# Kernel tuning notes

Measured on AMD Instinct MI355X. Metric: run time of the kernel, lower is better.

The kernel has to match this reference:

```python
import jax, jax.numpy as jnp
import numpy as np

N_IN = 1048576
C = 64
VT_OUT = 262144


def setup_inputs() -> dict:
    key = jax.random.key(0)
    k1, k2, k3 = jax.random.split(key, 3)
    inputs = jax.random.normal(k1, (N_IN, C), dtype=jnp.float32)
    # per-vertex replacement counts (used as weights in avg pooling)
    vt_replace = jax.random.randint(k2, (N_IN,), 0, 4, dtype=jnp.int64)
    # map each input vertex to its decimated output vertex
    vt_map = jax.random.randint(k3, (N_IN,), 0, VT_OUT, dtype=jnp.int64)
    return {"inputs": inputs, "vt_replace": vt_replace, "vt_map": vt_map, "vt_out": VT_OUT}


def reference(inputs, vt_replace, vt_map, vt_out):
    # method == 'max': segmented max over groups of input vertices that
    # collapse onto the same output vertex. vt_map < 0 means the vertex is
    # dropped; route those to an extra trash segment and slice it off.
    valid = vt_map >= 0
    seg = jnp.where(valid, vt_map, vt_out)  # [N_in]
    out = jax.ops.segment_max(inputs, seg, num_segments=vt_out + 1)[:vt_out]
    # empty segments come back as -inf; zero them like the CUDA kernel's init
    return jnp.where(jnp.isneginf(out), jnp.zeros((), dtype=out.dtype), out)
```

## Files before the change

kernel.cpp:

```cpp
#include <hip/hip_runtime.h>


#define CCH 64
#define NEG_INF (-__builtin_huge_valf())

__global__ void head_init_kernel(int* __restrict__ head, int vt_out) {
    int i = blockIdx.x * blockDim.x + threadIdx.x;
    if (i < vt_out) head[i] = -1;
}

__global__ void list_build_kernel(const int* __restrict__ vt_map,
                                  int* __restrict__ head,
                                  int* __restrict__ next,
                                  int n_in, int vt_out) {
    int r = blockIdx.x * blockDim.x + threadIdx.x;
    if (r >= n_in) return;
    int seg = vt_map[r];
    if (seg < 0 || seg >= vt_out) return;
    next[r] = atomicExch(&head[seg], r);
}

__global__ void gather_max_kernel(const float* __restrict__ in,
                                  const int* __restrict__ head,
                                  const int* __restrict__ next,
                                  float* __restrict__ out, int vt_out) {
    int wave = blockIdx.x * 4 + (threadIdx.x >> 6);
    int lane = threadIdx.x & 63;
    if (wave >= vt_out) return;
    int r = head[wave];
    float m = NEG_INF;
    while (r >= 0) {
        m = fmaxf(m, in[(size_t)r * CCH + lane]);
        r = next[r];
    }
    out[(size_t)wave * CCH + lane] = (m == NEG_INF) ? 0.0f : m;
}

__device__ __forceinline__ unsigned enc_f32(float f) {
    unsigned u = __float_as_uint(f);
    return (u & 0x80000000u) ? ~u : (u | 0x80000000u);
}
__device__ __forceinline__ float dec_f32(unsigned u) {
    unsigned b = (u & 0x80000000u) ? (u & 0x7fffffffu) : ~u;
    return __uint_as_float(b);
}
static constexpr unsigned ENC_NEG_INF = 0x007FFFFFu;

__global__ void pool_init_kernel(uint4* __restrict__ out, int n4) {
    int i = blockIdx.x * blockDim.x + threadIdx.x;
    if (i < n4) out[i] = make_uint4(ENC_NEG_INF, ENC_NEG_INF, ENC_NEG_INF, ENC_NEG_INF);
}
__global__ void pool_scatter_kernel(const float4* __restrict__ in,
                                    const int* __restrict__ vt_map,
                                    unsigned* __restrict__ out,
                                    int n_in, int vt_out) {
    int t = blockIdx.x * blockDim.x + threadIdx.x;
    int row = t >> 4, g = t & 15;
    if (row >= n_in) return;
    int seg = vt_map[row];
    if (seg < 0 || seg >= vt_out) return;
    float4 v = in[row * 16 + g];
    unsigned* dst = out + (size_t)seg * CCH + g * 4;
    atomicMax(dst + 0, enc_f32(v.x));
    atomicMax(dst + 1, enc_f32(v.y));
    atomicMax(dst + 2, enc_f32(v.z));
    atomicMax(dst + 3, enc_f32(v.w));
}
__global__ void pool_decode_kernel(uint4* __restrict__ out, int n4) {
    int i = blockIdx.x * blockDim.x + threadIdx.x;
    if (i >= n4) return;
    uint4 u = out[i];
    float4 f;
    f.x = (u.x == ENC_NEG_INF) ? 0.0f : dec_f32(u.x);
    f.y = (u.y == ENC_NEG_INF) ? 0.0f : dec_f32(u.y);
    f.z = (u.z == ENC_NEG_INF) ? 0.0f : dec_f32(u.z);
    f.w = (u.w == ENC_NEG_INF) ? 0.0f : dec_f32(u.w);
    ((float4*)out)[i] = f;
}

extern "C" void kernel_launch(void* const* d_in, const int* in_sizes, int n_in_arr,
                              void* d_out, int out_size, void* d_ws, size_t ws_size,
                              hipStream_t stream) {
    const float* in     = (const float*)d_in[0];
    const int*   vt_map = (const int*)d_in[2];
    float*       out    = (float*)d_out;

    const int n_in   = in_sizes[0] / CCH;
    const int vt_out = out_size / CCH;
    const int B = 256;

    const size_t ws_needed = (size_t)(vt_out + n_in) * sizeof(int);
    if (ws_size >= ws_needed) {
        int* head = (int*)d_ws;
        int* next = head + vt_out;
        head_init_kernel<<<(vt_out + B - 1) / B, B, 0, stream>>>(head, vt_out);
        list_build_kernel<<<(n_in + B - 1) / B, B, 0, stream>>>(
            vt_map, head, next, n_in, vt_out);
        const int waves = vt_out;
        gather_max_kernel<<<(waves + 3) / 4, B, 0, stream>>>(
            in, head, next, out, vt_out);
    } else {
        unsigned* out_u = (unsigned*)d_out;
        const int n4 = out_size / 4;
        pool_init_kernel<<<(n4 + B - 1) / B, B, 0, stream>>>((uint4*)out_u, n4);
        pool_scatter_kernel<<<(n_in * 16 + B - 1) / B, B, 0, stream>>>(
            (const float4*)in, vt_map, out_u, n_in, vt_out);
        pool_decode_kernel<<<(n4 + B - 1) / B, B, 0, stream>>>((uint4*)out_u, n4);
    }
}
```

Measured before the change: 489.2 us.

## Replace linked-list segment gather with CSR build and batched row loads

```diff
diff --git a/kernel.cpp b/kernel.cpp
--- a/kernel.cpp
+++ b/kernel.cpp
@@ -4,14 +4,120 @@
 #define CCH 64
 #define NEG_INF (-__builtin_huge_valf())
 
+
+__global__ void zero_kernel(int* __restrict__ p, int n) {
+    int i = blockIdx.x * blockDim.x + threadIdx.x;
+    if (i < n) p[i] = 0;
+}
+
+__global__ void count_kernel(const int* __restrict__ vt_map,
+                             int* __restrict__ cnt,
+                             int* __restrict__ rank,
+                             int n_in, int vt_out) {
+    int r = blockIdx.x * blockDim.x + threadIdx.x;
+    if (r >= n_in) return;
+    int seg = vt_map[r];
+    if (seg < 0 || seg >= vt_out) { rank[r] = -1; return; }
+    rank[r] = atomicAdd(&cnt[seg], 1);
+}
+
+__global__ void bsum_kernel(const int* __restrict__ cnt, int* __restrict__ bs,
+                            int vt_out) {
+    __shared__ int s[256];
+    int b = blockIdx.x, t = threadIdx.x, i = b * 256 + t;
+    s[t] = (i < vt_out) ? cnt[i] : 0;
+    __syncthreads();
+    for (int d = 128; d > 0; d >>= 1) {
+        if (t < d) s[t] += s[t + d];
+        __syncthreads();
+    }
+    if (t == 0) bs[b] = s[0];
+}
+
+__global__ void scan_bs_kernel(int* __restrict__ bs, int n) {
+    __shared__ int s[1024];
+    int t = threadIdx.x;
+    s[t] = (t < n) ? bs[t] : 0;
+    __syncthreads();
+    for (int d = 1; d < 1024; d <<= 1) {
+        int x = (t >= d) ? s[t - d] : 0;
+        __syncthreads();
+        s[t] += x;
+        __syncthreads();
+    }
+    if (t < n) bs[t] = (t == 0) ? 0 : s[t - 1];
+}
+
+__global__ void offsets_kernel(const int* __restrict__ cnt,
+                               const int* __restrict__ bs,
+                               int* __restrict__ offs, int vt_out) {
+    __shared__ int s[256];
+    int b = blockIdx.x, t = threadIdx.x, i = b * 256 + t;
+    int v = (i < vt_out) ? cnt[i] : 0;
+    s[t] = v;
+    __syncthreads();
+    for (int d = 1; d < 256; d <<= 1) {
+        int x = (t >= d) ? s[t - d] : 0;
+        __syncthreads();
+        s[t] += x;
+        __syncthreads();
+    }
+    int excl = (t == 0) ? 0 : s[t - 1];
+    if (i < vt_out) offs[i] = bs[b] + excl;
+}
+
+__global__ void place_kernel(const int* __restrict__ vt_map,
+                             const int* __restrict__ rank,
+                             const int* __restrict__ offs,
+                             int* __restrict__ idx, int n_in, int vt_out) {
+    int r = blockIdx.x * blockDim.x + threadIdx.x;
+    if (r >= n_in) return;
+    int seg = vt_map[r];
+    if (seg < 0 || seg >= vt_out) return;
+    idx[offs[seg] + rank[r]] = r;
+}
+
+__global__ __launch_bounds__(256) void csr_gather_kernel(
+        const float* __restrict__ in,
+        const int* __restrict__ cnt,
+        const int* __restrict__ offs,
+        const int* __restrict__ idx,
+        float* __restrict__ out, int vt_out) {
+    int wave = blockIdx.x * 4 + (threadIdx.x >> 6);
+    int lane = threadIdx.x & 63;
+    if (wave >= vt_out) return;
+    int c = cnt[wave];
+    int o = offs[wave];
+    float m = NEG_INF;
+    while (c > 0) {
+        int take = (c < 64) ? c : 64;
+        int rvec = idx[o + ((lane < take) ? lane : (take - 1))];
+        for (int j = 0; j < take; j += 8) {
+            float v[8];
+#pragma unroll
+            for (int k = 0; k < 8; ++k) {
+                int t = j + k;
+                int rk = __shfl(rvec, (t < take) ? t : (take - 1), 64);
+                v[k] = in[(size_t)rk * CCH + lane];
+            }
+#pragma unroll
+            for (int k = 0; k < 8; ++k) {
+                if (j + k < take) m = fmaxf(m, v[k]);
+            }
+        }
+        o += take;
+        c -= take;
+    }
+    out[(size_t)wave * CCH + lane] = (m == NEG_INF) ? 0.0f : m;
+}
+
+
 __global__ void head_init_kernel(int* __restrict__ head, int vt_out) {
     int i = blockIdx.x * blockDim.x + threadIdx.x;
     if (i < vt_out) head[i] = -1;
 }
-
 __global__ void list_build_kernel(const int* __restrict__ vt_map,
-                                  int* __restrict__ head,
-                                  int* __restrict__ next,
+                                  int* __restrict__ head, int* __restrict__ next,
                                   int n_in, int vt_out) {
     int r = blockIdx.x * blockDim.x + threadIdx.x;
     if (r >= n_in) return;
@@ -19,7 +125,6 @@
     if (seg < 0 || seg >= vt_out) return;
     next[r] = atomicExch(&head[seg], r);
 }
-
 __global__ void gather_max_kernel(const float* __restrict__ in,
                                   const int* __restrict__ head,
                                   const int* __restrict__ next,
@@ -36,6 +141,7 @@
     out[(size_t)wave * CCH + lane] = (m == NEG_INF) ? 0.0f : m;
 }
 
+
 __device__ __forceinline__ unsigned enc_f32(float f) {
     unsigned u = __float_as_uint(f);
     return (u & 0x80000000u) ? ~u : (u | 0x80000000u);
@@ -52,8 +158,7 @@
 }
 __global__ void pool_scatter_kernel(const float4* __restrict__ in,
                                     const int* __restrict__ vt_map,
-                                    unsigned* __restrict__ out,
-                                    int n_in, int vt_out) {
+                                    unsigned* __restrict__ out, int n_in, int vt_out) {
     int t = blockIdx.x * blockDim.x + threadIdx.x;
     int row = t >> 4, g = t & 15;
     if (row >= n_in) return;
@@ -78,6 +183,7 @@
     ((float4*)out)[i] = f;
 }
 
+
 extern "C" void kernel_launch(void* const* d_in, const int* in_sizes, int n_in_arr,
                               void* d_out, int out_size, void* d_ws, size_t ws_size,
                               hipStream_t stream) {
@@ -88,17 +194,31 @@
     const int n_in   = in_sizes[0] / CCH;
     const int vt_out = out_size / CCH;
     const int B = 256;
-
-    const size_t ws_needed = (size_t)(vt_out + n_in) * sizeof(int);
-    if (ws_size >= ws_needed) {
+    const int nblk = (vt_out + 255) / 256;
+
+    const size_t ws_csr = ((size_t)vt_out * 2 + (size_t)n_in * 2 + nblk) * sizeof(int);
+    const size_t ws_ll  = (size_t)(vt_out + n_in) * sizeof(int);
+
+    if (ws_size >= ws_csr && nblk <= 1024) {
+        int* cnt  = (int*)d_ws;
+        int* offs = cnt + vt_out;
+        int* rank = offs + vt_out;
+        int* idx  = rank + n_in;
+        int* bs   = idx + n_in;
+
+        zero_kernel<<<(vt_out + B - 1) / B, B, 0, stream>>>(cnt, vt_out);
+        count_kernel<<<(n_in + B - 1) / B, B, 0, stream>>>(vt_map, cnt, rank, n_in, vt_out);
+        bsum_kernel<<<nblk, 256, 0, stream>>>(cnt, bs, vt_out);
+        scan_bs_kernel<<<1, 1024, 0, stream>>>(bs, nblk);
+        offsets_kernel<<<nblk, 256, 0, stream>>>(cnt, bs, offs, vt_out);
+        place_kernel<<<(n_in + B - 1) / B, B, 0, stream>>>(vt_map, rank, offs, idx, n_in, vt_out);
+        csr_gather_kernel<<<(vt_out + 3) / 4, B, 0, stream>>>(in, cnt, offs, idx, out, vt_out);
+    } else if (ws_size >= ws_ll) {
         int* head = (int*)d_ws;
         int* next = head + vt_out;
         head_init_kernel<<<(vt_out + B - 1) / B, B, 0, stream>>>(head, vt_out);
-        list_build_kernel<<<(n_in + B - 1) / B, B, 0, stream>>>(
-            vt_map, head, next, n_in, vt_out);
-        const int waves = vt_out;
-        gather_max_kernel<<<(waves + 3) / 4, B, 0, stream>>>(
-            in, head, next, out, vt_out);
+        list_build_kernel<<<(n_in + B - 1) / B, B, 0, stream>>>(vt_map, head, next, n_in, vt_out);
+        gather_max_kernel<<<(vt_out + 3) / 4, B, 0, stream>>>(in, head, next, out, vt_out);
     } else {
         unsigned* out_u = (unsigned*)d_out;
         const int n4 = out_size / 4;
```

Measured after the change: 485.8 us. About the same (-0.7%).

## Replace linked-list segment gather with fixed-capacity buckets and overflow list

Applied to the files above, without the earlier changes.

```diff
diff --git a/kernel.cpp b/kernel.cpp
--- a/kernel.cpp
+++ b/kernel.cpp
@@ -2,39 +2,95 @@
 
 
 #define CCH 64
+#define CAP 16
 #define NEG_INF (-__builtin_huge_valf())
 
-__global__ void head_init_kernel(int* __restrict__ head, int vt_out) {
+__global__ void zero_kernel(int* __restrict__ p, int n) {
     int i = blockIdx.x * blockDim.x + threadIdx.x;
-    if (i < vt_out) head[i] = -1;
+    if (i < n) p[i] = 0;
 }
 
-__global__ void list_build_kernel(const int* __restrict__ vt_map,
-                                  int* __restrict__ head,
-                                  int* __restrict__ next,
-                                  int n_in, int vt_out) {
+__global__ void count_place_kernel(const int* __restrict__ vt_map,
+                                   int* __restrict__ cnt,
+                                   int* __restrict__ idx,
+                                   int* __restrict__ ovf_n,
+                                   int* __restrict__ ovf_rows,
+                                   int n_in, int vt_out) {
     int r = blockIdx.x * blockDim.x + threadIdx.x;
     if (r >= n_in) return;
     int seg = vt_map[r];
     if (seg < 0 || seg >= vt_out) return;
-    next[r] = atomicExch(&head[seg], r);
+    int slot = atomicAdd(&cnt[seg], 1);
+    if (slot < CAP) {
+        idx[seg * CAP + slot] = r;
+    } else {
+        int e = atomicAdd(ovf_n, 1);
+        ovf_rows[e] = r;
+    }
 }
 
-__global__ void gather_max_kernel(const float* __restrict__ in,
-                                  const int* __restrict__ head,
-                                  const int* __restrict__ next,
-                                  float* __restrict__ out, int vt_out) {
-    int wave = blockIdx.x * 4 + (threadIdx.x >> 6);
+__global__ __launch_bounds__(256) void bucket_gather_kernel(
+        const float4* __restrict__ in4,
+        const int* __restrict__ cnt,
+        const int* __restrict__ idx,
+        const int* __restrict__ ovf_n,
+        const int* __restrict__ ovf_rows,
+        const int* __restrict__ vt_map,
+        float4* __restrict__ out4, int vt_out) {
+    int wid  = blockIdx.x * 4 + (threadIdx.x >> 6);
     int lane = threadIdx.x & 63;
-    if (wave >= vt_out) return;
-    int r = head[wave];
-    float m = NEG_INF;
-    while (r >= 0) {
-        m = fmaxf(m, in[(size_t)r * CCH + lane]);
-        r = next[r];
+    int sub  = lane >> 4;
+    int g    = lane & 15;
+    int seg  = wid * 4 + sub;
+    if (seg >= vt_out) return;
+
+    int c  = cnt[seg];
+    int rv = idx[seg * CAP + g];
+    int cc = (c < CAP) ? c : CAP;
+
+    float4 m = make_float4(NEG_INF, NEG_INF, NEG_INF, NEG_INF);
+    for (int j = 0; j < cc; j += 4) {
+        float4 v[4];
+#pragma unroll
+        for (int k = 0; k < 4; ++k) {
+            int t  = j + k;
+            int tt = (t < cc) ? t : (cc - 1);
+            int rid = __shfl(rv, (sub << 4) + tt, 64);
+            v[k] = in4[(size_t)rid * 16 + g];
+        }
+#pragma unroll
+        for (int k = 0; k < 4; ++k) {
+            if (j + k < cc) {
+                m.x = fmaxf(m.x, v[k].x);
+                m.y = fmaxf(m.y, v[k].y);
+                m.z = fmaxf(m.z, v[k].z);
+                m.w = fmaxf(m.w, v[k].w);
+            }
+        }
     }
-    out[(size_t)wave * CCH + lane] = (m == NEG_INF) ? 0.0f : m;
+
+    if (c > CAP) {
+        int ne = *ovf_n;
+        for (int e = 0; e < ne; ++e) {
+            int r = ovf_rows[e];
+            if (vt_map[r] == seg) {
+                float4 v = in4[(size_t)r * 16 + g];
+                m.x = fmaxf(m.x, v.x);
+                m.y = fmaxf(m.y, v.y);
+                m.z = fmaxf(m.z, v.z);
+                m.w = fmaxf(m.w, v.w);
+            }
+        }
+    }
+
+    float4 o;
+    o.x = (m.x == NEG_INF) ? 0.0f : m.x;
+    o.y = (m.y == NEG_INF) ? 0.0f : m.y;
+    o.z = (m.z == NEG_INF) ? 0.0f : m.z;
+    o.w = (m.w == NEG_INF) ? 0.0f : m.w;
+    out4[(size_t)seg * 16 + g] = o;
 }
+
 
 __device__ __forceinline__ unsigned enc_f32(float f) {
     unsigned u = __float_as_uint(f);
@@ -52,8 +108,7 @@
 }
 __global__ void pool_scatter_kernel(const float4* __restrict__ in,
                                     const int* __restrict__ vt_map,
-                                    unsigned* __restrict__ out,
-                                    int n_in, int vt_out) {
+                                    unsigned* __restrict__ out, int n_in, int vt_out) {
     int t = blockIdx.x * blockDim.x + threadIdx.x;
     int row = t >> 4, g = t & 15;
     if (row >= n_in) return;
@@ -78,6 +133,7 @@
     ((float4*)out)[i] = f;
 }
 
+
 extern "C" void kernel_launch(void* const* d_in, const int* in_sizes, int n_in_arr,
                               void* d_out, int out_size, void* d_ws, size_t ws_size,
                               hipStream_t stream) {
@@ -89,16 +145,22 @@
     const int vt_out = out_size / CCH;
     const int B = 256;
 
-    const size_t ws_needed = (size_t)(vt_out + n_in) * sizeof(int);
+    const size_t ws_needed =
+        ((size_t)vt_out * (CAP + 1) + 1 + (size_t)n_in) * sizeof(int);
+
     if (ws_size >= ws_needed) {
-        int* head = (int*)d_ws;
-        int* next = head + vt_out;
-        head_init_kernel<<<(vt_out + B - 1) / B, B, 0, stream>>>(head, vt_out);
-        list_build_kernel<<<(n_in + B - 1) / B, B, 0, stream>>>(
-            vt_map, head, next, n_in, vt_out);
-        const int waves = vt_out;
-        gather_max_kernel<<<(waves + 3) / 4, B, 0, stream>>>(
-            in, head, next, out, vt_out);
+        int* cnt      = (int*)d_ws;
+        int* ovf_n    = cnt + vt_out;
+        int* idx      = ovf_n + 1;
+        int* ovf_rows = idx + (size_t)vt_out * CAP;
+
+        zero_kernel<<<(vt_out + 1 + B - 1) / B, B, 0, stream>>>(cnt, vt_out + 1);
+        count_place_kernel<<<(n_in + B - 1) / B, B, 0, stream>>>(
+            vt_map, cnt, idx, ovf_n, ovf_rows, n_in, vt_out);
+        const int nwave = (vt_out + 3) / 4;
+        bucket_gather_kernel<<<(nwave + 3) / 4, B, 0, stream>>>(
+            (const float4*)in, cnt, idx, ovf_n, ovf_rows, vt_map,
+            (float4*)out, vt_out);
     } else {
         unsigned* out_u = (unsigned*)d_out;
         const int n4 = out_size / 4;
```

Result: faster. 470.0 us (-3.9%).
